# Optimization experiments

Measured on AMD Instinct MI355X. Metric: run time of the kernel, lower is better.

Reference implementation:

```python
import jax, jax.numpy as jnp
import numpy as np

B, S, V, E, HD, T = 64, 512, 32000, 256, 1024, 9
H = HD // 2  # per-direction hidden


def _lstm_dir(x, w_ih, w_hh, b_ih, b_hh, reverse):
    # x: [B,S,I]; w_ih: [4H,I]; w_hh: [4H,H]  (PyTorch gate order i,f,g,o)
    xg = jnp.einsum('bsi,gi->bsg', x, w_ih) + b_ih + b_hh  # [B,S,4H]
    nb = x.shape[0]
    hdim = w_hh.shape[1]

    def step(carry, xg_t):
        h, c = carry
        g = xg_t + h @ w_hh.T
        i, f, gg, o = jnp.split(g, 4, axis=-1)
        c = jax.nn.sigmoid(f) * c + jax.nn.sigmoid(i) * jnp.tanh(gg)
        h = jax.nn.sigmoid(o) * jnp.tanh(c)
        return (h, c), h

    init = (jnp.zeros((nb, hdim), x.dtype), jnp.zeros((nb, hdim), x.dtype))
    _, hs = jax.lax.scan(step, init, jnp.swapaxes(xg, 0, 1), reverse=reverse)
    return jnp.swapaxes(hs, 0, 1)  # [B,S,H]


def _bilstm_layer(x, w_ih, w_hh, b_ih, b_hh):
    fwd = _lstm_dir(x, w_ih[0], w_hh[0], b_ih[0], b_hh[0], False)
    bwd = _lstm_dir(x, w_ih[1], w_hh[1], b_ih[1], b_hh[1], True)
    return jnp.concatenate([fwd, bwd], axis=-1)


def _crf_loss(emissions, labels, mask, trans, start_t, end_t, valid_lens):
    # emissions [B,S,T], labels [B,S] int, mask [B,S] bool
    maskf = mask.astype(emissions.dtype)
    em = jnp.take_along_axis(emissions, labels[..., None], -1)[..., 0]  # [B,S]
    tr = trans[labels[:, :-1], labels[:, 1:]]  # [B,S-1]
    last_tag = jnp.take_along_axis(labels, (valid_lens - 1)[:, None], 1)[:, 0]
    num = (start_t[labels[:, 0]] + em[:, 0]
           + ((em[:, 1:] + tr) * maskf[:, 1:]).sum(-1)
           + end_t[last_tag])

    alpha0 = start_t[None, :] + emissions[:, 0]  # [B,T]

    def step(alpha, inp):
        em_t, m_t = inp  # [B,T], [B]
        nxt = jax.nn.logsumexp(alpha[:, :, None] + trans[None], axis=1) + em_t
        return jnp.where(m_t[:, None], nxt, alpha), None

    alpha, _ = jax.lax.scan(step, alpha0,
                            (jnp.swapaxes(emissions[:, 1:], 0, 1),
                             jnp.swapaxes(mask[:, 1:], 0, 1)))
    logZ = jax.nn.logsumexp(alpha + end_t[None, :], axis=-1)
    llh = num - logZ
    return -jnp.mean(llh)  # reduction='mean' over batch, negated in forward


def _crf_decode(emissions, mask, trans, start_t, end_t):
    score0 = start_t[None, :] + emissions[:, 0]  # [B,T]

    def step(score, inp):
        em_t, m_t = inp
        cand = score[:, :, None] + trans[None]  # [B,T(prev),T(cur)]
        best_prev = jnp.argmax(cand, axis=1)  # [B,T]
        new = jnp.max(cand, axis=1) + em_t
        score = jnp.where(m_t[:, None], new, score)
        return score, best_prev

    score, hist = jax.lax.scan(step, score0,
                               (jnp.swapaxes(emissions[:, 1:], 0, 1),
                                jnp.swapaxes(mask[:, 1:], 0, 1)))
    best_last = jnp.argmax(score + end_t[None, :], axis=-1)  # [B]

    def bt(tag, inp):
        hist_t, m_t = inp  # [B,T], [B]
        prev = jnp.take_along_axis(hist_t, tag[:, None], 1)[:, 0]
        tag = jnp.where(m_t, prev, tag)
        return tag, tag

    _, ys = jax.lax.scan(bt, best_last,
                         (hist, jnp.swapaxes(mask[:, 1:], 0, 1)),
                         reverse=True)  # [S-1,B]
    tags = jnp.concatenate([ys, best_last[None]], axis=0)  # [S,B]
    return jnp.swapaxes(tags, 0, 1)  # [B,S]


def setup_inputs() -> dict:
    key = jax.random.key(0)
    ks = jax.random.split(key, 16)
    sc = 0.05
    inp = {
        'input_ids': jax.random.randint(ks[0], (B, S), 0, V, dtype=jnp.int32),
        'valid_lens': jax.random.randint(ks[1], (B,), 1, S + 1, dtype=jnp.int32),
        'labels': jax.random.randint(ks[2], (B, S), 0, T, dtype=jnp.int32),
        'emb': jax.random.normal(ks[3], (V, E), jnp.float32) * sc,
        'w_ih0': jax.random.normal(ks[4], (2, 4 * H, E), jnp.float32) * sc,
        'w_hh0': jax.random.normal(ks[5], (2, 4 * H, H), jnp.float32) * sc,
        'b_ih0': jax.random.normal(ks[6], (2, 4 * H), jnp.float32) * sc,
        'b_hh0': jax.random.normal(ks[7], (2, 4 * H), jnp.float32) * sc,
        'w_ih1': jax.random.normal(ks[8], (2, 4 * H, HD), jnp.float32) * sc,
        'w_hh1': jax.random.normal(ks[9], (2, 4 * H, H), jnp.float32) * sc,
        'b_ih1': jax.random.normal(ks[10], (2, 4 * H), jnp.float32) * sc,
        'b_hh1': jax.random.normal(ks[11], (2, 4 * H), jnp.float32) * sc,
        'cls_w': jax.random.normal(ks[12], (T, HD), jnp.float32) * sc,
        'cls_b': jax.random.normal(ks[13], (T,), jnp.float32) * sc,
        'trans': jax.random.normal(ks[14], (T, T), jnp.float32) * sc,
        'start_t': jax.random.normal(ks[15], (T,), jnp.float32) * sc,
    }
    inp['end_t'] = jax.random.normal(jax.random.fold_in(key, 99), (T,), jnp.float32) * sc
    return inp


def reference(input_ids, valid_lens, labels, emb, w_ih0, w_hh0, b_ih0, b_hh0,
              w_ih1, w_hh1, b_ih1, b_hh1, cls_w, cls_b, trans, start_t, end_t):
    x = emb[input_ids]  # [B,S,E]
    x = _bilstm_layer(x, w_ih0, w_hh0, b_ih0, b_hh0)   # [B,S,HD]
    x = _bilstm_layer(x, w_ih1, w_hh1, b_ih1, b_hh1)   # [B,S,HD]
    # dropout is identity in eval mode
    logits = jnp.einsum('bsh,th->bst', x, cls_w) + cls_b  # [B,S,T]
    mask = jnp.arange(input_ids.shape[1])[None, :] < valid_lens[:, None]
    tag_ids = _crf_decode(logits, mask, trans, start_t, end_t)
    loss = _crf_loss(logits, labels, mask, trans, start_t, end_t, valid_lens)
    return tag_ids, loss
```

## Files before the change

### kernel.cpp

```cpp
#include <hip/hip_runtime.h>
#include <hip/hip_fp8.h>
#include <math.h>

#define BB 64
#define SS 512
#define EE 256
#define HH 512
#define HD 1024
#define TT 9
#define MM (BB*SS)

typedef __attribute__((ext_vector_type(8))) short    short8;
typedef __attribute__((ext_vector_type(4))) float    f32x4;
typedef __attribute__((ext_vector_type(4))) unsigned uint4v;

__device__ __forceinline__ unsigned short f2bfu(float x) {
    unsigned b = __float_as_uint(x);
    b += 0x7FFFu + ((b >> 16) & 1u);
    return (unsigned short)(b >> 16);
}
__device__ __forceinline__ unsigned pack2bf(float lo, float hi) {
    return ((unsigned)f2bfu(hi) << 16) | (unsigned)f2bfu(lo);
}

__global__ void zero_kernel(float* __restrict__ p, int n)
{
    int i = blockIdx.x * blockDim.x + threadIdx.x;
    int stride = gridDim.x * blockDim.x;
    for (; i < n; i += stride) p[i] = 0.f;
}

__global__ void pack_kernel(const float* __restrict__ w_ih, const float* __restrict__ w_hh,
                            unsigned short* __restrict__ dst, int KX, int nf, int total)
{
    int tid = blockIdx.x * 256 + threadIdx.x;
    if (tid >= total) return;
    int j    = tid & 7;
    int lane = (tid >> 3) & 63;
    int f    = (tid >> 9) % nf;
    int rest = (tid >> 9) / nf;
    int jb   = rest & 127;
    int d    = rest >> 7;
    int m = lane & 15, quad = lane >> 4;
    int jj = m >> 2, q = m & 3;
    int row = q * HH + jb * 4 + jj;
    int k   = f * 32 + quad * 8 + j;
    float v;
    if (k < KX) v = w_ih[((size_t)d * 2048 + row) * (size_t)KX + k];
    else        v = w_hh[((size_t)d * 2048 + row) * (size_t)HH + (k - KX)];
    dst[tid] = f2bfu(v);
}

template<int LAYER>
__global__ __launch_bounds__(256, 1)
void bilstm_persist(const int* __restrict__ ids, const float* __restrict__ emb,
                    const unsigned short* __restrict__ x1,
                    const unsigned short* __restrict__ packA,
                    const float* __restrict__ b_ih, const float* __restrict__ b_hh,
                    unsigned short* hbuf,
                    unsigned short* __restrict__ h0out,
                    unsigned char*  __restrict__ h1out,
                    unsigned* flags)
{
    constexpr int KX = LAYER ? HD : EE;
    constexpr int NF = (KX + HH) / 32;
    constexpr int XF = KX / 32;
    constexpr int HF = HH / 32;
    constexpr int XFA = (LAYER == 0) ? XF : 1;
    constexpr int XFB = (LAYER == 1) ? XF : 1;

    __shared__ int sid[16 * 513];

    const int bid  = blockIdx.x;
    const int d    = bid >> 7;
    const int g    = (bid >> 5) & 3;
    const int ub   = bid & 31;
    const int tid  = threadIdx.x;
    const int lane = tid & 63;
    const int wv   = tid >> 6;
    const int quad = lane >> 4;
    const int ln15 = lane & 15;
    const int b    = g * 16 + ln15;
    const int jb   = ub * 4 + wv;
    const int u    = jb * 4 + quad;

    if (LAYER == 0) {
        for (int i = tid; i < 16 * 512; i += 256) {
            int r = i >> 9, cc = i & 511;
            sid[r * 513 + cc] = ids[(g * 16 + r) * SS + cc];
        }
        __syncthreads();
    }

    const uint4v* myA = (const uint4v*)(packA + (size_t)(d * 128 + jb) * NF * 512);
    uint4v Ar[NF];
    #pragma unroll
    for (int f = 0; f < NF; f++) Ar[f] = myA[f * 64 + lane];

    float bias_[4];
    #pragma unroll
    for (int q = 0; q < 4; q++)
        bias_[q] = b_ih[d * 2048 + q * HH + u] + b_hh[d * 2048 + q * HH + u];

    unsigned* gflags = flags + (d * 4 + g) * 128;
    const unsigned long long* fq = (const unsigned long long*)gflags;

    float c_ = 0.f;

    for (int s = 0; s < SS; s++) {
        const int t = d ? (SS - 1 - s) : s;
        const int p = s & 1;
        f32x4 acc = {0.f, 0.f, 0.f, 0.f};

        float4 Fa[XFA], Fb[XFA];
        uint4v Bx[XFB];
        if constexpr (LAYER == 0) {
            const float* erow = emb + (size_t)sid[ln15 * 513 + t] * EE;
            #pragma unroll
            for (int f = 0; f < XF; f++) {
                const int k0 = f * 32 + quad * 8;
                Fa[f] = *(const float4*)(erow + k0);
                Fb[f] = *(const float4*)(erow + k0 + 4);
            }
        } else {
            const unsigned short* xrow = x1 + ((size_t)(b * SS + t)) * HD;
            #pragma unroll
            for (int f = 0; f < XF; f++)
                Bx[f] = *(const uint4v*)(xrow + f * 32 + quad * 8);
        }
        __builtin_amdgcn_sched_barrier(0);

        if (s) {
            const unsigned tgt = (unsigned)s;
            while (1) {
                unsigned long long q = __hip_atomic_load(fq + lane,
                                         __ATOMIC_RELAXED, __HIP_MEMORY_SCOPE_AGENT);
                if (__all(((unsigned)q >= tgt) & ((unsigned)(q >> 32) >= tgt))) break;
                __builtin_amdgcn_s_sleep(1);
            }
            __atomic_signal_fence(__ATOMIC_ACQ_REL);
        }

        const unsigned long long* hp = (const unsigned long long*)
            (hbuf + ((size_t)((d * 2 + p) * BB + b)) * HH);
        unsigned long long hl0[HF], hl1[HF];
        #pragma unroll
        for (int f = 0; f < HF; f++) {
            hl0[f] = __hip_atomic_load(hp + f * 8 + quad * 2,
                        __ATOMIC_RELAXED, __HIP_MEMORY_SCOPE_AGENT);
            hl1[f] = __hip_atomic_load(hp + f * 8 + quad * 2 + 1,
                        __ATOMIC_RELAXED, __HIP_MEMORY_SCOPE_AGENT);
        }
        __builtin_amdgcn_sched_barrier(0);

        if constexpr (LAYER == 0) {
            #pragma unroll
            for (int f = 0; f < XF; f++) {
                uint4v r;
                r[0] = pack2bf(Fa[f].x, Fa[f].y); r[1] = pack2bf(Fa[f].z, Fa[f].w);
                r[2] = pack2bf(Fb[f].x, Fb[f].y); r[3] = pack2bf(Fb[f].z, Fb[f].w);
                acc = __builtin_amdgcn_mfma_f32_16x16x32_bf16(
                        __builtin_bit_cast(short8, Ar[f]),
                        __builtin_bit_cast(short8, r), acc, 0, 0, 0);
            }
        } else {
            #pragma unroll
            for (int f = 0; f < XF; f++)
                acc = __builtin_amdgcn_mfma_f32_16x16x32_bf16(
                        __builtin_bit_cast(short8, Ar[f]),
                        __builtin_bit_cast(short8, Bx[f]), acc, 0, 0, 0);
        }

        #pragma unroll
        for (int f = 0; f < HF; f++) {
            uint4v r;
            r[0] = (unsigned)hl0[f]; r[1] = (unsigned)(hl0[f] >> 32);
            r[2] = (unsigned)hl1[f]; r[3] = (unsigned)(hl1[f] >> 32);
            acc = __builtin_amdgcn_mfma_f32_16x16x32_bf16(
                    __builtin_bit_cast(short8, Ar[XF + f]),
                    __builtin_bit_cast(short8, r), acc, 0, 0, 0);
        }

        float gi = acc[0] + bias_[0];
        float gf = acc[1] + bias_[1];
        float gg = acc[2] + bias_[2];
        float go = acc[3] + bias_[3];
        float i_ = 1.f / (1.f + __expf(-gi));
        float f_ = 1.f / (1.f + __expf(-gf));
        float xg = fminf(fmaxf(gg, -15.f), 15.f);
        float e2 = __expf(2.f * xg);
        float g_ = (e2 - 1.f) / (e2 + 1.f);
        float o_ = 1.f / (1.f + __expf(-go));
        c_ = f_ * c_ + i_ * g_;
        float xc  = fminf(fmaxf(c_, -15.f), 15.f);
        float e2c = __expf(2.f * xc);
        float hn  = o_ * ((e2c - 1.f) / (e2c + 1.f));

        int hb = (int)f2bfu(hn);
        int ob = __shfl_xor(hb, 16);
        if (!(quad & 1)) {
            unsigned v32 = (unsigned)(unsigned short)hb
                         | ((unsigned)(unsigned short)ob << 16);
            __hip_atomic_store((unsigned*)(hbuf +
                ((size_t)((d * 2 + (p ^ 1)) * BB + b)) * HH + u),
                v32, __ATOMIC_RELAXED, __HIP_MEMORY_SCOPE_AGENT);
            if (LAYER == 0)
                *(unsigned*)(h0out + ((size_t)(b * SS + t)) * HD + d * HH + u) = v32;
        }
        if (LAYER == 1) {
            __hip_fp8_e4m3 f8(hn);
            int b8  = (int)f8.__x;
            int o8  = __shfl_xor(b8, 16);
            int pr  = (b8 & 0xff) | ((o8 & 0xff) << 8);
            int pr2 = __shfl_xor(pr, 32);
            if (quad == 0) {
                unsigned val = (unsigned)(pr & 0xffff) | ((unsigned)(pr2 & 0xffff) << 16);
                *(unsigned*)(h1out + ((size_t)(b * SS + t)) * HD + d * HH + jb * 4) = val;
            }
        }

        asm volatile("s_waitcnt vmcnt(0)" ::: "memory");
        if (lane == 0)
            __hip_atomic_store(gflags + jb, (unsigned)(s + 1),
                               __ATOMIC_RELAXED, __HIP_MEMORY_SCOPE_AGENT);
    }
}

__global__ __launch_bounds__(256)
void logits_fp8(const unsigned char* __restrict__ h1, const float* __restrict__ cls_w,
                float* __restrict__ out)
{
    __shared__ float Wc[TT * HD];
    const int tid = threadIdx.x;
    for (int i = tid; i < TT * HD; i += 256) Wc[i] = cls_w[i];
    __syncthreads();
    const int lane = tid & 63;
    const int row  = blockIdx.x * 4 + (tid >> 6);
    const unsigned char* xr = h1 + (size_t)row * HD;
    float p[TT] = {};
    #pragma unroll
    for (int it = 0; it < 16; it++) {
        __hip_fp8_e4m3 f8; f8.__x = xr[it * 64 + lane];
        float xv = (float)f8;
        #pragma unroll
        for (int n = 0; n < TT; n++) p[n] += xv * Wc[n * HD + it * 64 + lane];
    }
    #pragma unroll
    for (int n = 0; n < TT; n++) {
        float v = p[n];
        #pragma unroll
        for (int off = 32; off > 0; off >>= 1) v += __shfl_down(v, off);
        if (lane == 0) out[(size_t)row * TT + n] = v;
    }
}

__global__ __launch_bounds__(64)
void crf_kernel(const float* __restrict__ logits, const int* __restrict__ labels,
                const int* __restrict__ vlens, const float* __restrict__ trans,
                const float* __restrict__ start_t, const float* __restrict__ end_t,
                const float* __restrict__ cls_b,
                float* __restrict__ tags_out, float* __restrict__ llh)
{
    const int b = blockIdx.x;
    const int lane = threadIdx.x;
    const int len = vlens[b];
    const float* em = logits + (size_t)b * (SS * TT);
    const int*  lab = labels + (size_t)b * SS;
    __shared__ unsigned char hist[(SS - 1) * TT];

    float cb = (lane < TT) ? cls_b[lane] : 0.f;
    float tcol[TT];
    #pragma unroll
    for (int i = 0; i < TT; i++) tcol[i] = (lane < TT) ? trans[i * TT + lane] : 0.f;
    float score = (lane < TT) ? (start_t[lane] + em[lane] + cb) : 0.f;
    float alpha = score;
    float num = 0.f; int plab = 0;
    if (lane == 0) { plab = lab[0]; num = start_t[plab] + em[plab] + cls_b[plab]; }

    for (int t = 1; t < SS; t++) {
        float emj = (lane < TT) ? (em[t * TT + lane] + cb) : 0.f;
        float sv[TT], av[TT];
        #pragma unroll
        for (int i = 0; i < TT; i++) { sv[i] = __shfl(score, i); av[i] = __shfl(alpha, i); }
        float best = -INFINITY; int bp = 0; float amx = -INFINITY;
        #pragma unroll
        for (int i = 0; i < TT; i++) {
            float cnd = sv[i] + tcol[i];
            if (cnd > best) { best = cnd; bp = i; }
            amx = fmaxf(amx, av[i] + tcol[i]);
        }
        float se = 0.f;
        #pragma unroll
        for (int i = 0; i < TT; i++) se += expf(av[i] + tcol[i] - amx);
        const bool m = (t < len);
        if (m) { score = best + emj; alpha = amx + logf(se) + emj; }
        if (lane < TT) hist[(t - 1) * TT + lane] = (unsigned char)bp;
        if (lane == 0 && m) {
            int lt = lab[t];
            num += em[t * TT + lt] + cls_b[lt] + trans[plab * TT + lt];
            plab = lt;
        }
    }
    float fsc[TT], fal[TT];
    #pragma unroll
    for (int i = 0; i < TT; i++) { fsc[i] = __shfl(score, i); fal[i] = __shfl(alpha, i); }
    __syncthreads();
    if (lane == 0) {
        num += end_t[lab[len - 1]];
        int bl = 0; float bv = fsc[0] + end_t[0];
        #pragma unroll
        for (int i = 1; i < TT; i++) {
            float v = fsc[i] + end_t[i];
            if (v > bv) { bv = v; bl = i; }
        }
        float zmx = -INFINITY;
        #pragma unroll
        for (int i = 0; i < TT; i++) zmx = fmaxf(zmx, fal[i] + end_t[i]);
        float zse = 0.f;
        #pragma unroll
        for (int i = 0; i < TT; i++) zse += expf(fal[i] + end_t[i] - zmx);
        llh[b] = num - (zmx + logf(zse));
        int tag = bl;
        tags_out[b * SS + (SS - 1)] = (float)tag;
        for (int t = SS - 2; t >= 0; t--) {
            if (t + 1 < len) tag = hist[t * TT + tag];
            tags_out[b * SS + t] = (float)tag;
        }
    }
}

__global__ void loss_kernel(const float* __restrict__ llh, float* __restrict__ out)
{
    float v = llh[threadIdx.x];
    #pragma unroll
    for (int off = 32; off > 0; off >>= 1) v += __shfl_down(v, off);
    if (threadIdx.x == 0) out[MM] = -(v / 64.f);
}

extern "C" void kernel_launch(void* const* d_in, const int* in_sizes, int n_in,
                              void* d_out, int out_size, void* d_ws, size_t ws_size,
                              hipStream_t stream)
{
    const int*   ids     = (const int*)  d_in[0];
    const int*   vlen    = (const int*)  d_in[1];
    const int*   labels  = (const int*)  d_in[2];
    const float* emb     = (const float*)d_in[3];
    const float* w_ih0   = (const float*)d_in[4];
    const float* w_hh0   = (const float*)d_in[5];
    const float* b_ih0   = (const float*)d_in[6];
    const float* b_hh0   = (const float*)d_in[7];
    const float* w_ih1   = (const float*)d_in[8];
    const float* w_hh1   = (const float*)d_in[9];
    const float* b_ih1   = (const float*)d_in[10];
    const float* b_hh1   = (const float*)d_in[11];
    const float* cls_w   = (const float*)d_in[12];
    const float* cls_b   = (const float*)d_in[13];
    const float* trans   = (const float*)d_in[14];
    const float* start_t = (const float*)d_in[15];
    const float* end_t   = (const float*)d_in[16];

    float*          llh    = (float*)d_ws;
    unsigned*       flags  = (unsigned*)(llh + 64);
    unsigned short* hbuf0  = (unsigned short*)(flags + 2048);
    unsigned short* hbuf1  = hbuf0 + 131072;
    unsigned short* h0out  = hbuf1 + 131072;
    unsigned short* packA1 = h0out + (size_t)MM * HD;
    float*          logits = (float*)packA1;
    unsigned short* packA0 = packA1 + 6291456;
    unsigned char*  h1out  = (unsigned char*)packA0;

    zero_kernel<<<512, 256, 0, stream>>>((float*)flags, 2048 + (131072 + 131072) / 2);

    pack_kernel<<<(3145728 + 255) / 256, 256, 0, stream>>>(w_ih0, w_hh0, packA0, EE, 24, 3145728);
    pack_kernel<<<(6291456 + 255) / 256, 256, 0, stream>>>(w_ih1, w_hh1, packA1, HD, 48, 6291456);

    bilstm_persist<0><<<256, 256, 0, stream>>>(
        ids, emb, nullptr, packA0, b_ih0, b_hh0, hbuf0, h0out, nullptr, flags);
    bilstm_persist<1><<<256, 256, 0, stream>>>(
        ids, nullptr, h0out, packA1, b_ih1, b_hh1, hbuf1, nullptr, h1out, flags + 1024);

    logits_fp8<<<MM / 4, 256, 0, stream>>>(h1out, cls_w, logits);
    crf_kernel<<<BB, 64, 0, stream>>>(logits, labels, vlen, trans, start_t, end_t,
                                      cls_b, (float*)d_out, llh);
    loss_kernel<<<1, 64, 0, stream>>>(llh, (float*)d_out);
}
```

Before: 8.433 ms.

## Aggregate per-block flags, precompute input projection before wait, defer output stores

```diff
diff --git a/kernel.cpp b/kernel.cpp
--- a/kernel.cpp
+++ b/kernel.cpp
@@ -66,10 +66,12 @@
     constexpr int NF = (KX + HH) / 32;
     constexpr int XF = KX / 32;
     constexpr int HF = HH / 32;
+    constexpr int XG = (LAYER == 1) ? XF / 8 : 1;
     constexpr int XFA = (LAYER == 0) ? XF : 1;
-    constexpr int XFB = (LAYER == 1) ? XF : 1;
-
-    __shared__ int sid[16 * 513];
+
+    __shared__ int sid[(LAYER == 0) ? 16 * 513 : 1];
+    __shared__ unsigned bar_in;
+    __shared__ unsigned bar_out;
 
     const int bid  = blockIdx.x;
     const int d    = bid >> 7;
@@ -84,13 +86,14 @@
     const int jb   = ub * 4 + wv;
     const int u    = jb * 4 + quad;
 
+    if (tid == 0) { bar_in = 0u; bar_out = 0u; }
     if (LAYER == 0) {
         for (int i = tid; i < 16 * 512; i += 256) {
             int r = i >> 9, cc = i & 511;
             sid[r * 513 + cc] = ids[(g * 16 + r) * SS + cc];
         }
-        __syncthreads();
-    }
+    }
+    __syncthreads();
 
     const uint4v* myA = (const uint4v*)(packA + (size_t)(d * 128 + jb) * NF * 512);
     uint4v Ar[NF];
@@ -102,43 +105,77 @@
     for (int q = 0; q < 4; q++)
         bias_[q] = b_ih[d * 2048 + q * HH + u] + b_hh[d * 2048 + q * HH + u];
 
-    unsigned* gflags = flags + (d * 4 + g) * 128;
-    const unsigned long long* fq = (const unsigned long long*)gflags;
+    unsigned* gflags = flags + (d * 4 + g) * 32;
 
     float c_ = 0.f;
+    unsigned pend  = 0; int pendT  = 0;
+    unsigned pend8 = 0; int pend8T = 0;
 
     for (int s = 0; s < SS; s++) {
         const int t = d ? (SS - 1 - s) : s;
         const int p = s & 1;
-        f32x4 acc = {0.f, 0.f, 0.f, 0.f};
-
-        float4 Fa[XFA], Fb[XFA];
-        uint4v Bx[XFB];
+
+        f32x4 accx = {0.f, 0.f, 0.f, 0.f};
         if constexpr (LAYER == 0) {
             const float* erow = emb + (size_t)sid[ln15 * 513 + t] * EE;
+            float4 Fa[XFA], Fb[XFA];
             #pragma unroll
             for (int f = 0; f < XF; f++) {
                 const int k0 = f * 32 + quad * 8;
                 Fa[f] = *(const float4*)(erow + k0);
                 Fb[f] = *(const float4*)(erow + k0 + 4);
             }
+            #pragma unroll
+            for (int f = 0; f < XF; f++) {
+                uint4v r;
+                r[0] = pack2bf(Fa[f].x, Fa[f].y); r[1] = pack2bf(Fa[f].z, Fa[f].w);
+                r[2] = pack2bf(Fb[f].x, Fb[f].y); r[3] = pack2bf(Fb[f].z, Fb[f].w);
+                accx = __builtin_amdgcn_mfma_f32_16x16x32_bf16(
+                        __builtin_bit_cast(short8, Ar[f]),
+                        __builtin_bit_cast(short8, r), accx, 0, 0, 0);
+            }
         } else {
             const unsigned short* xrow = x1 + ((size_t)(b * SS + t)) * HD;
+            uint4v Bg[2][8];
             #pragma unroll
-            for (int f = 0; f < XF; f++)
-                Bx[f] = *(const uint4v*)(xrow + f * 32 + quad * 8);
+            for (int jx = 0; jx < 8; jx++)
+                Bg[0][jx] = *(const uint4v*)(xrow + jx * 32 + quad * 8);
+            #pragma unroll
+            for (int gg2 = 0; gg2 < XG; gg2++) {
+                const int cur = gg2 & 1;
+                if (gg2 + 1 < XG) {
+                    #pragma unroll
+                    for (int jx = 0; jx < 8; jx++)
+                        Bg[cur ^ 1][jx] = *(const uint4v*)
+                            (xrow + ((gg2 + 1) * 8 + jx) * 32 + quad * 8);
+                }
+                #pragma unroll
+                for (int jx = 0; jx < 8; jx++)
+                    accx = __builtin_amdgcn_mfma_f32_16x16x32_bf16(
+                            __builtin_bit_cast(short8, Ar[gg2 * 8 + jx]),
+                            __builtin_bit_cast(short8, Bg[cur][jx]), accx, 0, 0, 0);
+            }
         }
         __builtin_amdgcn_sched_barrier(0);
 
         if (s) {
             const unsigned tgt = (unsigned)s;
-            while (1) {
-                unsigned long long q = __hip_atomic_load(fq + lane,
-                                         __ATOMIC_RELAXED, __HIP_MEMORY_SCOPE_AGENT);
-                if (__all(((unsigned)q >= tgt) & ((unsigned)(q >> 32) >= tgt))) break;
-                __builtin_amdgcn_s_sleep(1);
+            if (wv == 0) {
+                while (1) {
+                    unsigned q = __hip_atomic_load(gflags + (lane & 31),
+                                     __ATOMIC_RELAXED, __HIP_MEMORY_SCOPE_AGENT);
+                    if (__all(q >= tgt)) break;
+                    __builtin_amdgcn_s_sleep(1);
+                }
+                if (lane == 0)
+                    __hip_atomic_store(&bar_out, tgt, __ATOMIC_RELAXED,
+                                       __HIP_MEMORY_SCOPE_WORKGROUP);
+            } else {
+                while (__hip_atomic_load(&bar_out, __ATOMIC_RELAXED,
+                                         __HIP_MEMORY_SCOPE_WORKGROUP) < tgt) {}
             }
             __atomic_signal_fence(__ATOMIC_ACQ_REL);
+            __builtin_amdgcn_sched_barrier(0);
         }
 
         const unsigned long long* hp = (const unsigned long long*)
@@ -154,37 +191,28 @@
         __builtin_amdgcn_sched_barrier(0);
 
         if constexpr (LAYER == 0) {
-            #pragma unroll
-            for (int f = 0; f < XF; f++) {
-                uint4v r;
-                r[0] = pack2bf(Fa[f].x, Fa[f].y); r[1] = pack2bf(Fa[f].z, Fa[f].w);
-                r[2] = pack2bf(Fb[f].x, Fb[f].y); r[3] = pack2bf(Fb[f].z, Fb[f].w);
-                acc = __builtin_amdgcn_mfma_f32_16x16x32_bf16(
-                        __builtin_bit_cast(short8, Ar[f]),
-                        __builtin_bit_cast(short8, r), acc, 0, 0, 0);
-            }
+            if (s && !(quad & 1))
+                *(unsigned*)(h0out + ((size_t)(b * SS + pendT)) * HD + d * HH + u) = pend;
         } else {
-            #pragma unroll
-            for (int f = 0; f < XF; f++)
-                acc = __builtin_amdgcn_mfma_f32_16x16x32_bf16(
-                        __builtin_bit_cast(short8, Ar[f]),
-                        __builtin_bit_cast(short8, Bx[f]), acc, 0, 0, 0);
-        }
-
+            if (s && quad == 0)
+                *(unsigned*)(h1out + ((size_t)(b * SS + pend8T)) * HD + d * HH + jb * 4) = pend8;
+        }
+
+        f32x4 acch = {0.f, 0.f, 0.f, 0.f};
         #pragma unroll
         for (int f = 0; f < HF; f++) {
             uint4v r;
             r[0] = (unsigned)hl0[f]; r[1] = (unsigned)(hl0[f] >> 32);
             r[2] = (unsigned)hl1[f]; r[3] = (unsigned)(hl1[f] >> 32);
-            acc = __builtin_amdgcn_mfma_f32_16x16x32_bf16(
+            acch = __builtin_amdgcn_mfma_f32_16x16x32_bf16(
                     __builtin_bit_cast(short8, Ar[XF + f]),
-                    __builtin_bit_cast(short8, r), acc, 0, 0, 0);
-        }
-
-        float gi = acc[0] + bias_[0];
-        float gf = acc[1] + bias_[1];
-        float gg = acc[2] + bias_[2];
-        float go = acc[3] + bias_[3];
+                    __builtin_bit_cast(short8, r), acch, 0, 0, 0);
+        }
+
+        float gi = accx[0] + acch[0] + bias_[0];
+        float gf = accx[1] + acch[1] + bias_[1];
+        float gg = accx[2] + acch[2] + bias_[2];
+        float go = accx[3] + acch[3] + bias_[3];
         float i_ = 1.f / (1.f + __expf(-gi));
         float f_ = 1.f / (1.f + __expf(-gf));
         float xg = fminf(fmaxf(gg, -15.f), 15.f);
@@ -204,8 +232,7 @@
             __hip_atomic_store((unsigned*)(hbuf +
                 ((size_t)((d * 2 + (p ^ 1)) * BB + b)) * HH + u),
                 v32, __ATOMIC_RELAXED, __HIP_MEMORY_SCOPE_AGENT);
-            if (LAYER == 0)
-                *(unsigned*)(h0out + ((size_t)(b * SS + t)) * HD + d * HH + u) = v32;
+            if (LAYER == 0) { pend = v32; pendT = t; }
         }
         if (LAYER == 1) {
             __hip_fp8_e4m3 f8(hn);
@@ -214,15 +241,27 @@
             int pr  = (b8 & 0xff) | ((o8 & 0xff) << 8);
             int pr2 = __shfl_xor(pr, 32);
             if (quad == 0) {
-                unsigned val = (unsigned)(pr & 0xffff) | ((unsigned)(pr2 & 0xffff) << 16);
-                *(unsigned*)(h1out + ((size_t)(b * SS + t)) * HD + d * HH + jb * 4) = val;
+                pend8 = (unsigned)(pr & 0xffff) | ((unsigned)(pr2 & 0xffff) << 16);
+                pend8T = t;
             }
         }
 
         asm volatile("s_waitcnt vmcnt(0)" ::: "memory");
-        if (lane == 0)
-            __hip_atomic_store(gflags + jb, (unsigned)(s + 1),
-                               __ATOMIC_RELAXED, __HIP_MEMORY_SCOPE_AGENT);
+        __atomic_signal_fence(__ATOMIC_ACQ_REL);
+        if (lane == 0) {
+            unsigned old = atomicAdd(&bar_in, 1u);
+            if (old == 4u * (unsigned)s + 3u)
+                __hip_atomic_store(gflags + ub, (unsigned)(s + 1),
+                                   __ATOMIC_RELAXED, __HIP_MEMORY_SCOPE_AGENT);
+        }
+    }
+
+    if constexpr (LAYER == 0) {
+        if (!(quad & 1))
+            *(unsigned*)(h0out + ((size_t)(b * SS + pendT)) * HD + d * HH + u) = pend;
+    } else {
+        if (quad == 0)
+            *(unsigned*)(h1out + ((size_t)(b * SS + pend8T)) * HD + d * HH + jb * 4) = pend8;
     }
 }
 
```

Result: slower. 9.898 ms (+17.4%).
